# Performance work log

Hardware: AMD Instinct MI355X
Metric: run time of the kernel (lower is better)

The kernel has to match this reference:

```python
import jax, jax.numpy as jnp
import numpy as np


def setup_inputs() -> dict:
    key = jax.random.key(0)
    k1, k2 = jax.random.split(key)
    B, Ld, Lq, D = 32, 2048, 512, 256
    doc = jax.random.normal(k1, (B, Ld, D), dtype=jnp.float32)
    query = jax.random.normal(k2, (B, Lq, D), dtype=jnp.float32)
    doc_mask = jnp.ones((B, Ld), dtype=jnp.float32)
    q_mask = jnp.ones((B, Lq), dtype=jnp.float32)
    return {"doc": doc, "query": query, "doc_mask": doc_mask, "q_mask": q_mask}


def reference(doc, query, doc_mask, q_mask):
    # match_score: [B, Lq, Ld] = tanh(query @ doc^T)
    match_score = jnp.tanh(jnp.einsum('bqd,btd->bqt', query, doc))
    # sum over query positions -> [B, Ld]; softmax over doc positions
    query_to_doc_att = jax.nn.softmax(jnp.sum(match_score, axis=1), axis=-1)
    # sum over doc positions -> [B, Lq]; softmax over query positions
    doc_to_query_att = jax.nn.softmax(jnp.sum(match_score, axis=-1), axis=-1)
    # mask and renormalize
    alpha = query_to_doc_att * doc_mask
    alpha = alpha / jnp.sum(alpha, axis=1, keepdims=True)
    beta = doc_to_query_att * q_mask
    beta = beta / jnp.sum(beta, axis=1, keepdims=True)
    # weighted pooling: doc^T @ alpha -> [B, D]; query^T @ beta -> [B, D]
    doc_vector = jnp.einsum('btd,bt->bd', doc, alpha)
    que_vector = jnp.einsum('bqd,bq->bd', query, beta)
    return jnp.concatenate([doc_vector, que_vector], axis=1)  # [B, 2D]
```

## Files before the change

### kernel.cpp

```cpp
#include <hip/hip_runtime.h>
#include <hip/hip_bf16.h>
#include <cstdint>

#define BB 32
#define LD 2048
#define LQ 512
#define DD 256
#define BM 256
#define BN 256
#define BK 64

typedef _Float16 half8 __attribute__((ext_vector_type(8)));
typedef _Float16 half4 __attribute__((ext_vector_type(4)));
typedef float float4v __attribute__((ext_vector_type(4)));

__device__ __forceinline__ float tanh_fast(float x) {
    float t = __builtin_amdgcn_exp2f(x * 2.885390081777927f);
    float r = __builtin_amdgcn_rcpf(t + 1.0f);
    return fmaf(-2.0f, r, 1.0f);
}

__global__ __launch_bounds__(512, 2) void k1(const float* __restrict__ qsrc,
                                             const float* __restrict__ dsrc,
                                             float* __restrict__ pa,
                                             float* __restrict__ pb) {
    __shared__ _Float16 sQ[BM * BK];
    __shared__ _Float16 sD[BN * BK];
    __shared__ float srow[BM][4];
    __shared__ float scol[BN][2];
    const int bq = blockIdx.x, bt = blockIdx.y, b = blockIdx.z;
    const int tid = threadIdx.x;
    const int lane = tid & 63;
    const int wave = tid >> 6;
    const int r16 = lane & 15;
    const int q4 = lane >> 4;
    const int wr = wave >> 2, wc = wave & 3;
    const int mb = wr * 128, nb = wc * 64;

    float4v acc[8][4];
    float4v zero = {0.f, 0.f, 0.f, 0.f};
#pragma unroll
    for (int m = 0; m < 8; m++)
#pragma unroll
        for (int n = 0; n < 4; n++) acc[m][n] = zero;

    const int r0 = tid >> 4;
    const int c = tid & 15;
    const int c2 = c >> 1, hlf = c & 1;
    const int p = c2 ^ (r0 & 7);
    const int ldsoff = r0 * BK + p * 8 + hlf * 4;
    const float* Qf = qsrc + ((size_t)b * LQ + bq * BM + r0) * DD + 4 * c;
    const float* Df = dsrc + ((size_t)b * LD + bt * BN + r0) * DD + 4 * c;

    for (int kk = 0; kk < DD; kk += BK) {
        __syncthreads();
#pragma unroll
        for (int i = 0; i < 8; i++) {
            float4v v = *(const float4v*)(Qf + kk + (size_t)i * 32 * DD);
            half4 h = {(_Float16)v[0], (_Float16)v[1], (_Float16)v[2], (_Float16)v[3]};
            *(half4*)(&sQ[ldsoff + i * 32 * BK]) = h;
            float4v w = *(const float4v*)(Df + kk + (size_t)i * 32 * DD);
            half4 h2 = {(_Float16)w[0], (_Float16)w[1], (_Float16)w[2], (_Float16)w[3]};
            *(half4*)(&sD[ldsoff + i * 32 * BK]) = h2;
        }
        __syncthreads();

#pragma unroll
        for (int kk2 = 0; kk2 < 2; kk2++) {
            const int sw = ((4 * kk2 + q4) ^ (r16 & 7)) * 8;
            half8 af[8], bf[4];
#pragma unroll
            for (int m = 0; m < 8; m++) af[m] = *(const half8*)(&sQ[(mb + 16 * m + r16) * BK + sw]);
#pragma unroll
            for (int n = 0; n < 4; n++) bf[n] = *(const half8*)(&sD[(nb + 16 * n + r16) * BK + sw]);
#pragma unroll
            for (int m = 0; m < 8; m++)
#pragma unroll
                for (int n = 0; n < 4; n++)
                    acc[m][n] = __builtin_amdgcn_mfma_f32_16x16x32_f16(af[m], bf[n], acc[m][n], 0, 0, 0);
        }
    }

    float rsum[8][4];
    float csum[4];
#pragma unroll
    for (int m = 0; m < 8; m++)
#pragma unroll
        for (int r = 0; r < 4; r++) rsum[m][r] = 0.f;
#pragma unroll
    for (int n = 0; n < 4; n++) csum[n] = 0.f;

#pragma unroll
    for (int m = 0; m < 8; m++)
#pragma unroll
        for (int n = 0; n < 4; n++) {
            float t0 = tanh_fast(acc[m][n][0]);
            float t1 = tanh_fast(acc[m][n][1]);
            float t2 = tanh_fast(acc[m][n][2]);
            float t3 = tanh_fast(acc[m][n][3]);
            csum[n] += t0 + t1 + t2 + t3;
            rsum[m][0] += t0;
            rsum[m][1] += t1;
            rsum[m][2] += t2;
            rsum[m][3] += t3;
        }

#pragma unroll
    for (int m = 0; m < 8; m++) {
#pragma unroll
        for (int r = 0; r < 4; r++) {
            float v = rsum[m][r];
            v += __shfl_xor(v, 1);
            v += __shfl_xor(v, 2);
            v += __shfl_xor(v, 4);
            v += __shfl_xor(v, 8);
            rsum[m][r] = v;
        }
        if (r16 < 4) {
            float v = (r16 == 0) ? rsum[m][0] : (r16 == 1) ? rsum[m][1] : (r16 == 2) ? rsum[m][2] : rsum[m][3];
            srow[mb + 16 * m + 4 * q4 + r16][wc] = v;
        }
    }
#pragma unroll
    for (int n = 0; n < 4; n++) {
        float v = csum[n];
        v += __shfl_xor(v, 16);
        v += __shfl_xor(v, 32);
        if (lane < 16) scol[nb + 16 * n + lane][wr] = v;
    }
    __syncthreads();
    if (tid < 256) {
        float v = srow[tid][0] + srow[tid][1] + srow[tid][2] + srow[tid][3];
        pb[((size_t)bt * BB + b) * LQ + bq * BM + tid] = v;
        float u = scol[tid][0] + scol[tid][1];
        pa[((size_t)bq * BB + b) * LD + bt * BN + tid] = u;
    }
}

__global__ __launch_bounds__(256) void k2(const float* __restrict__ pa, const float* __restrict__ pb,
                                          const float* __restrict__ dmask, const float* __restrict__ qmask,
                                          float* __restrict__ alpha, float* __restrict__ beta,
                                          float* __restrict__ out) {
    __shared__ float sl[2048];
    __shared__ float sm[4], ss[4];
    int blk = blockIdx.x, tid = threadIdx.x, lane = tid & 63, wave = tid >> 6;
    const float* mk;
    float* dst;
    int n;
    if (blk < BB) {
        int b = blk;
        out[b * 2 * DD + tid] = 0.f;
        out[b * 2 * DD + 256 + tid] = 0.f;
        n = LD;
        mk = dmask + b * LD;
        dst = alpha + b * LD;
        for (int i = tid; i < n; i += 256)
            sl[i] = pa[(size_t)b * LD + i] + pa[((size_t)BB + b) * LD + i];
    } else {
        int b = blk - BB;
        n = LQ;
        mk = qmask + b * LQ;
        dst = beta + b * LQ;
        for (int i = tid; i < n; i += 256) {
            float s = 0.f;
#pragma unroll
            for (int bt = 0; bt < 8; bt++) s += pb[((size_t)bt * BB + b) * LQ + i];
            sl[i] = s;
        }
    }
    __syncthreads();
    float mx = -3.0e38f;
    for (int i = tid; i < n; i += 256) mx = fmaxf(mx, sl[i]);
#pragma unroll
    for (int s = 1; s < 64; s <<= 1) mx = fmaxf(mx, __shfl_xor(mx, s));
    if (lane == 0) sm[wave] = mx;
    __syncthreads();
    mx = fmaxf(fmaxf(sm[0], sm[1]), fmaxf(sm[2], sm[3]));
    const float L2E = 1.4426950408889634f;
    float sum = 0.f;
    for (int i = tid; i < n; i += 256) {
        float e = __builtin_amdgcn_exp2f((sl[i] - mx) * L2E) * mk[i];
        sl[i] = e;
        sum += e;
    }
#pragma unroll
    for (int s = 1; s < 64; s <<= 1) sum += __shfl_xor(sum, s);
    if (lane == 0) ss[wave] = sum;
    __syncthreads();
    sum = ss[0] + ss[1] + ss[2] + ss[3];
    float inv = 1.0f / sum;
    for (int i = tid; i < n; i += 256) dst[i] = sl[i] * inv;
}

__global__ __launch_bounds__(256) void k3(const float* __restrict__ docf, const float* __restrict__ qryf,
                                          const float* __restrict__ alpha, const float* __restrict__ beta,
                                          float* __restrict__ out) {
    __shared__ float sm[8 * DD];
    int blk = blockIdx.x, tid = threadIdx.x;
    const float* srcf;
    const float* w;
    float* dst;
    if (blk < BB * 16) {
        int b = blk >> 4, ch = blk & 15;
        srcf = docf + ((size_t)b * LD + ch * 128) * DD;
        w = alpha + b * LD + ch * 128;
        dst = out + b * 2 * DD;
    } else {
        int k = blk - BB * 16;
        int b = k >> 2, ch = k & 3;
        srcf = qryf + ((size_t)b * LQ + ch * 128) * DD;
        w = beta + b * LQ + ch * 128;
        dst = out + b * 2 * DD + DD;
    }
    int g = tid >> 5, c = tid & 31;
    float acc[8];
#pragma unroll
    for (int j = 0; j < 8; j++) acc[j] = 0.f;
    for (int r = 0; r < 16; r++) {
        int t = r * 8 + g;
        float wt = w[t];
        const float4v* p = (const float4v*)(srcf + (size_t)t * DD + c * 8);
        float4v x0 = p[0], x1 = p[1];
#pragma unroll
        for (int j = 0; j < 4; j++) { acc[j] += wt * x0[j]; acc[4 + j] += wt * x1[j]; }
    }
#pragma unroll
    for (int j = 0; j < 8; j++) sm[g * DD + c * 8 + j] = acc[j];
    __syncthreads();
    float s = 0.f;
#pragma unroll
    for (int g2 = 0; g2 < 8; g2++) s += sm[g2 * DD + tid];
    atomicAdd(dst + tid, s);
}

extern "C" void kernel_launch(void* const* d_in, const int* in_sizes, int n_in,
                              void* d_out, int out_size, void* d_ws, size_t ws_size,
                              hipStream_t stream) {
    (void)in_sizes; (void)n_in; (void)out_size; (void)ws_size;
    const float* doc = (const float*)d_in[0];
    const float* qry = (const float*)d_in[1];
    const float* dmask = (const float*)d_in[2];
    const float* qmask = (const float*)d_in[3];
    float* out = (float*)d_out;

    float* pa = (float*)d_ws;
    float* pb = pa + 2 * BB * LD;
    float* alpha = pb + 8 * BB * LQ;
    float* beta = alpha + BB * LD;

    k1<<<dim3(LQ / BM, LD / BN, BB), 512, 0, stream>>>(qry, doc, pa, pb);
    k2<<<2 * BB, 256, 0, stream>>>(pa, pb, dmask, qmask, alpha, beta, out);
    k3<<<BB * 16 + BB * 4, 256, 0, stream>>>(doc, qry, alpha, beta, out);
}
```

Before: 165.8 us.

## Shrink GEMM tiles to 128x128 with register-prefetched global loads

The fused matmul+tanh kernel now uses 128x128 tiles with 256 threads (4 waves, 4x4 MFMA tiles each) instead of 256x256 with 512 threads. The next K-slice is prefetched into registers while MFMAs run on the current LDS tile, so global load latency overlaps compute. Partial-sum buffers grow, and the softmax kernel now reduces 4 doc partials and 16 query partials. Smaller tiles give more blocks and lower register pressure, but each block reuses loaded data less and the global fp32 input traffic doubles. The pooling loop is also unrolled.

```diff
diff --git a/kernel.cpp b/kernel.cpp
--- a/kernel.cpp
+++ b/kernel.cpp
@@ -6,8 +6,8 @@
 #define LD 2048
 #define LQ 512
 #define DD 256
-#define BM 256
-#define BN 256
+#define BM 128
+#define BN 128
 #define BK 64
 
 typedef _Float16 half8 __attribute__((ext_vector_type(8)));
@@ -20,13 +20,13 @@
     return fmaf(-2.0f, r, 1.0f);
 }
 
-__global__ __launch_bounds__(512, 2) void k1(const float* __restrict__ qsrc,
-                                             const float* __restrict__ dsrc,
-                                             float* __restrict__ pa,
-                                             float* __restrict__ pb) {
+__global__ __launch_bounds__(256) void k1(const float* __restrict__ qsrc,
+                                          const float* __restrict__ dsrc,
+                                          float* __restrict__ pa,
+                                          float* __restrict__ pb) {
     __shared__ _Float16 sQ[BM * BK];
     __shared__ _Float16 sD[BN * BK];
-    __shared__ float srow[BM][4];
+    __shared__ float srow[BM][2];
     __shared__ float scol[BN][2];
     const int bq = blockIdx.x, bt = blockIdx.y, b = blockIdx.z;
     const int tid = threadIdx.x;
@@ -34,13 +34,12 @@
     const int wave = tid >> 6;
     const int r16 = lane & 15;
     const int q4 = lane >> 4;
-    const int wr = wave >> 2, wc = wave & 3;
-    const int mb = wr * 128, nb = wc * 64;
-
-    float4v acc[8][4];
+    const int mb = (wave >> 1) * 64, nb = (wave & 1) * 64;
+
+    float4v acc[4][4];
     float4v zero = {0.f, 0.f, 0.f, 0.f};
 #pragma unroll
-    for (int m = 0; m < 8; m++)
+    for (int m = 0; m < 4; m++)
 #pragma unroll
         for (int n = 0; n < 4; n++) acc[m][n] = zero;
 
@@ -52,46 +51,60 @@
     const float* Qf = qsrc + ((size_t)b * LQ + bq * BM + r0) * DD + 4 * c;
     const float* Df = dsrc + ((size_t)b * LD + bt * BN + r0) * DD + 4 * c;
 
-    for (int kk = 0; kk < DD; kk += BK) {
+    float4v rq[8], rd[8];
+#pragma unroll
+    for (int i = 0; i < 8; i++) {
+        rq[i] = *(const float4v*)(Qf + (size_t)i * 16 * DD);
+        rd[i] = *(const float4v*)(Df + (size_t)i * 16 * DD);
+    }
+
+    for (int kk4 = 0; kk4 < 4; kk4++) {
         __syncthreads();
 #pragma unroll
         for (int i = 0; i < 8; i++) {
-            float4v v = *(const float4v*)(Qf + kk + (size_t)i * 32 * DD);
-            half4 h = {(_Float16)v[0], (_Float16)v[1], (_Float16)v[2], (_Float16)v[3]};
-            *(half4*)(&sQ[ldsoff + i * 32 * BK]) = h;
-            float4v w = *(const float4v*)(Df + kk + (size_t)i * 32 * DD);
-            half4 h2 = {(_Float16)w[0], (_Float16)w[1], (_Float16)w[2], (_Float16)w[3]};
-            *(half4*)(&sD[ldsoff + i * 32 * BK]) = h2;
+            half4 h = {(_Float16)rq[i][0], (_Float16)rq[i][1], (_Float16)rq[i][2], (_Float16)rq[i][3]};
+            *(half4*)(&sQ[ldsoff + i * 16 * BK]) = h;
+            half4 h2 = {(_Float16)rd[i][0], (_Float16)rd[i][1], (_Float16)rd[i][2], (_Float16)rd[i][3]};
+            *(half4*)(&sD[ldsoff + i * 16 * BK]) = h2;
         }
         __syncthreads();
+
+        if (kk4 < 3) {
+            const int kk = (kk4 + 1) * BK;
+#pragma unroll
+            for (int i = 0; i < 8; i++) {
+                rq[i] = *(const float4v*)(Qf + kk + (size_t)i * 16 * DD);
+                rd[i] = *(const float4v*)(Df + kk + (size_t)i * 16 * DD);
+            }
+        }
 
 #pragma unroll
         for (int kk2 = 0; kk2 < 2; kk2++) {
             const int sw = ((4 * kk2 + q4) ^ (r16 & 7)) * 8;
-            half8 af[8], bf[4];
-#pragma unroll
-            for (int m = 0; m < 8; m++) af[m] = *(const half8*)(&sQ[(mb + 16 * m + r16) * BK + sw]);
+            half8 af[4], bf[4];
+#pragma unroll
+            for (int m = 0; m < 4; m++) af[m] = *(const half8*)(&sQ[(mb + 16 * m + r16) * BK + sw]);
 #pragma unroll
             for (int n = 0; n < 4; n++) bf[n] = *(const half8*)(&sD[(nb + 16 * n + r16) * BK + sw]);
 #pragma unroll
-            for (int m = 0; m < 8; m++)
+            for (int m = 0; m < 4; m++)
 #pragma unroll
                 for (int n = 0; n < 4; n++)
                     acc[m][n] = __builtin_amdgcn_mfma_f32_16x16x32_f16(af[m], bf[n], acc[m][n], 0, 0, 0);
         }
     }
 
-    float rsum[8][4];
+    float rsum[4][4];
     float csum[4];
 #pragma unroll
-    for (int m = 0; m < 8; m++)
+    for (int m = 0; m < 4; m++)
 #pragma unroll
         for (int r = 0; r < 4; r++) rsum[m][r] = 0.f;
 #pragma unroll
     for (int n = 0; n < 4; n++) csum[n] = 0.f;
 
 #pragma unroll
-    for (int m = 0; m < 8; m++)
+    for (int m = 0; m < 4; m++)
 #pragma unroll
         for (int n = 0; n < 4; n++) {
             float t0 = tanh_fast(acc[m][n][0]);
@@ -106,7 +119,7 @@
         }
 
 #pragma unroll
-    for (int m = 0; m < 8; m++) {
+    for (int m = 0; m < 4; m++) {
 #pragma unroll
         for (int r = 0; r < 4; r++) {
             float v = rsum[m][r];
@@ -118,7 +131,7 @@
         }
         if (r16 < 4) {
             float v = (r16 == 0) ? rsum[m][0] : (r16 == 1) ? rsum[m][1] : (r16 == 2) ? rsum[m][2] : rsum[m][3];
-            srow[mb + 16 * m + 4 * q4 + r16][wc] = v;
+            srow[mb + 16 * m + 4 * q4 + r16][wave & 1] = v;
         }
     }
 #pragma unroll
@@ -126,11 +139,11 @@
         float v = csum[n];
         v += __shfl_xor(v, 16);
         v += __shfl_xor(v, 32);
-        if (lane < 16) scol[nb + 16 * n + lane][wr] = v;
-    }
-    __syncthreads();
-    if (tid < 256) {
-        float v = srow[tid][0] + srow[tid][1] + srow[tid][2] + srow[tid][3];
+        if (lane < 16) scol[nb + 16 * n + lane][wave >> 1] = v;
+    }
+    __syncthreads();
+    if (tid < 128) {
+        float v = srow[tid][0] + srow[tid][1];
         pb[((size_t)bt * BB + b) * LQ + bq * BM + tid] = v;
         float u = scol[tid][0] + scol[tid][1];
         pa[((size_t)bq * BB + b) * LD + bt * BN + tid] = u;
@@ -154,8 +167,12 @@
         n = LD;
         mk = dmask + b * LD;
         dst = alpha + b * LD;
-        for (int i = tid; i < n; i += 256)
-            sl[i] = pa[(size_t)b * LD + i] + pa[((size_t)BB + b) * LD + i];
+        for (int i = tid; i < n; i += 256) {
+            float s = 0.f;
+#pragma unroll
+            for (int j = 0; j < 4; j++) s += pa[((size_t)j * BB + b) * LD + i];
+            sl[i] = s;
+        }
     } else {
         int b = blk - BB;
         n = LQ;
@@ -164,7 +181,7 @@
         for (int i = tid; i < n; i += 256) {
             float s = 0.f;
 #pragma unroll
-            for (int bt = 0; bt < 8; bt++) s += pb[((size_t)bt * BB + b) * LQ + i];
+            for (int j = 0; j < 16; j++) s += pb[((size_t)j * BB + b) * LQ + i];
             sl[i] = s;
         }
     }
@@ -216,6 +233,7 @@
     float acc[8];
 #pragma unroll
     for (int j = 0; j < 8; j++) acc[j] = 0.f;
+#pragma unroll
     for (int r = 0; r < 16; r++) {
         int t = r * 8 + g;
         float wt = w[t];
@@ -244,11 +262,11 @@
     float* out = (float*)d_out;
 
     float* pa = (float*)d_ws;
-    float* pb = pa + 2 * BB * LD;
-    float* alpha = pb + 8 * BB * LQ;
+    float* pb = pa + 4 * BB * LD;
+    float* alpha = pb + 16 * BB * LQ;
     float* beta = alpha + BB * LD;
 
-    k1<<<dim3(LQ / BM, LD / BN, BB), 512, 0, stream>>>(qry, doc, pa, pb);
+    k1<<<dim3(LQ / BM, LD / BN, BB), 256, 0, stream>>>(qry, doc, pa, pb);
     k2<<<2 * BB, 256, 0, stream>>>(pa, pb, dmask, qmask, alpha, beta, out);
     k3<<<BB * 16 + BB * 4, 256, 0, stream>>>(doc, qry, alpha, beta, out);
 }
```

Result: slower. 172.7 us (+4.2%).
